# Kernel optimization log

Measured on AMD Instinct MI355X. Metric: run time of the kernel, lower is better.

## Reference

```python
import jax, jax.numpy as jnp
import numpy as np

NUM_CLASSES = 50000
FEAT_DIM = 256
BATCH = 2048
CLAMP_MIN = 1e-12
CLAMP_MAX = 1e12


def setup_inputs() -> dict:
    key = jax.random.key(0)
    k1, k2, k3 = jax.random.split(key, 3)
    x = jax.random.normal(k1, (BATCH, FEAT_DIM), dtype=jnp.float32)
    labels = jax.random.randint(k2, (BATCH,), 0, NUM_CLASSES, dtype=jnp.int64)
    centers = jax.random.normal(k3, (NUM_CLASSES, FEAT_DIM), dtype=jnp.float32)
    class_weights = jnp.ones((NUM_CLASSES,), dtype=jnp.float32)
    return {"x": x, "centers": centers, "class_weights": class_weights, "labels": labels}


def reference(x, centers, class_weights, labels):
    # Original torch code builds a full (B, C) distmat via addmm, masks to the
    # true-class column, multiplies by class weights, clamps to [1e-12, 1e12],
    # and sums / B. Off-mask entries are exactly 0 -> clamped to 1e-12, so they
    # contribute a constant B*(C-1)*1e-12 to the sum. We compute the gathered
    # per-sample distance directly (same math) and add that constant, avoiding
    # the O(B*C) intermediate.
    B = x.shape[0]
    C = centers.shape[0]
    c = centers[labels]                                   # (B, D)
    d = (jnp.sum(x * x, axis=1)
         + jnp.sum(c * c, axis=1)
         - 2.0 * jnp.sum(x * c, axis=1))                  # (B,)
    w = class_weights[labels]                             # (B,)
    on_mask = jnp.clip(d * w, CLAMP_MIN, CLAMP_MAX)       # (B,)
    off_mask_const = jnp.float32(B * (C - 1)) * jnp.float32(CLAMP_MIN)
    loss = (jnp.sum(on_mask) + off_mask_const) / B
    return loss
```

## Files before the change

kernel.cpp:

```cpp
#include <hip/hip_runtime.h>


constexpr int B = 2048;
constexpr int D = 256;
constexpr int C = 50000;

__global__ __launch_bounds__(256) void wcl_persample(
    const float* __restrict__ x, const float* __restrict__ centers,
    const float* __restrict__ cw, const int* __restrict__ labels,
    float* __restrict__ partial) {
  const int lane = threadIdx.x & 63;
  const int wave = (int)((blockIdx.x * blockDim.x + threadIdx.x) >> 6);
  if (wave >= B) return;

  const int lbl = labels[wave];
  const float4 xv = reinterpret_cast<const float4*>(x + (size_t)wave * D)[lane];
  const float4 cv = reinterpret_cast<const float4*>(centers + (size_t)lbl * D)[lane];

  const float xx = xv.x * xv.x + xv.y * xv.y + xv.z * xv.z + xv.w * xv.w;
  const float cc = cv.x * cv.x + cv.y * cv.y + cv.z * cv.z + cv.w * cv.w;
  const float xc = xv.x * cv.x + xv.y * cv.y + xv.z * cv.z + xv.w * cv.w;
  float s = xx + cc - 2.0f * xc;

#pragma unroll
  for (int off = 32; off > 0; off >>= 1) s += __shfl_xor(s, off, 64);

  if (lane == 0) {
    float v = s * cw[lbl];
    v = fminf(fmaxf(v, 1e-12f), 1e12f);
    partial[wave] = v;
  }
}

__global__ __launch_bounds__(256) void wcl_reduce(
    const float* __restrict__ partial, float* __restrict__ out) {
  __shared__ float sdata[4];
  float s = 0.0f;
  for (int i = threadIdx.x; i < B; i += 256) s += partial[i];
#pragma unroll
  for (int off = 32; off > 0; off >>= 1) s += __shfl_xor(s, off, 64);
  const int wid = (int)(threadIdx.x >> 6);
  if ((threadIdx.x & 63) == 0) sdata[wid] = s;
  __syncthreads();
  if (threadIdx.x == 0) {
    const float tot = sdata[0] + sdata[1] + sdata[2] + sdata[3];
    const float off_const = (float)((double)B * (double)(C - 1)) * 1e-12f;
    out[0] = (tot + off_const) / (float)B;
  }
}

extern "C" void kernel_launch(void* const* d_in, const int* in_sizes, int n_in,
                              void* d_out, int out_size, void* d_ws, size_t ws_size,
                              hipStream_t stream) {
  const float* x       = (const float*)d_in[0];
  const float* centers = (const float*)d_in[1];
  const float* cw      = (const float*)d_in[2];
  const int*   labels  = (const int*)d_in[3];
  float* out = (float*)d_out;
  float* partial = (float*)d_ws;

  wcl_persample<<<(B * 64) / 256, 256, 0, stream>>>(x, centers, cw, labels, partial);
  wcl_reduce<<<1, 256, 0, stream>>>(partial, out);
}
```

Before: 13.31 us.

## Fuse per-sample and reduce kernels via cooperative grid sync

Merges the two launches into one cooperative kernel. Each block reduces its 8 samples into a block partial, then a grid-wide sync lets block 0 sum the 256 partials and write the loss. This removes a second kernel launch and the round trip through the partial buffer, at the cost of a grid barrier and the overhead of a cooperative launch.

```diff
diff --git a/kernel.cpp b/kernel.cpp
--- a/kernel.cpp
+++ b/kernel.cpp
@@ -1,51 +1,63 @@
 #include <hip/hip_runtime.h>
+#include <hip/hip_cooperative_groups.h>
+
+namespace cg = cooperative_groups;
 
 
 constexpr int B = 2048;
 constexpr int D = 256;
 constexpr int C = 50000;
+constexpr int BLOCKS = 256;
+constexpr int TPB = 512;
 
-__global__ __launch_bounds__(256) void wcl_persample(
+__global__ __launch_bounds__(TPB) void wcl_fused(
     const float* __restrict__ x, const float* __restrict__ centers,
     const float* __restrict__ cw, const int* __restrict__ labels,
-    float* __restrict__ partial) {
+    float* __restrict__ partial, float* __restrict__ out) {
+  __shared__ float sm[8];
   const int lane = threadIdx.x & 63;
-  const int wave = (int)((blockIdx.x * blockDim.x + threadIdx.x) >> 6);
-  if (wave >= B) return;
+  const int w = (int)(threadIdx.x >> 6);
+  const int s = (int)blockIdx.x * 8 + w;
 
-  const int lbl = labels[wave];
-  const float4 xv = reinterpret_cast<const float4*>(x + (size_t)wave * D)[lane];
+  const int lbl = labels[s];
+  const float4 xv = reinterpret_cast<const float4*>(x + (size_t)s * D)[lane];
   const float4 cv = reinterpret_cast<const float4*>(centers + (size_t)lbl * D)[lane];
 
   const float xx = xv.x * xv.x + xv.y * xv.y + xv.z * xv.z + xv.w * xv.w;
   const float cc = cv.x * cv.x + cv.y * cv.y + cv.z * cv.z + cv.w * cv.w;
   const float xc = xv.x * cv.x + xv.y * cv.y + xv.z * cv.z + xv.w * cv.w;
-  float s = xx + cc - 2.0f * xc;
+  float acc = xx + cc - 2.0f * xc;
 
 #pragma unroll
-  for (int off = 32; off > 0; off >>= 1) s += __shfl_xor(s, off, 64);
+  for (int off = 32; off > 0; off >>= 1) acc += __shfl_xor(acc, off, 64);
 
   if (lane == 0) {
-    float v = s * cw[lbl];
-    v = fminf(fmaxf(v, 1e-12f), 1e12f);
-    partial[wave] = v;
+    float v = acc * cw[lbl];
+    sm[w] = fminf(fmaxf(v, 1e-12f), 1e12f);
   }
-}
-
-__global__ __launch_bounds__(256) void wcl_reduce(
-    const float* __restrict__ partial, float* __restrict__ out) {
-  __shared__ float sdata[4];
-  float s = 0.0f;
-  for (int i = threadIdx.x; i < B; i += 256) s += partial[i];
-#pragma unroll
-  for (int off = 32; off > 0; off >>= 1) s += __shfl_xor(s, off, 64);
-  const int wid = (int)(threadIdx.x >> 6);
-  if ((threadIdx.x & 63) == 0) sdata[wid] = s;
   __syncthreads();
   if (threadIdx.x == 0) {
-    const float tot = sdata[0] + sdata[1] + sdata[2] + sdata[3];
-    const float off_const = (float)((double)B * (double)(C - 1)) * 1e-12f;
-    out[0] = (tot + off_const) / (float)B;
+    float t = 0.0f;
+#pragma unroll
+    for (int i = 0; i < 8; ++i) t += sm[i];
+    partial[blockIdx.x] = t;
+  }
+
+  cg::this_grid().sync();
+
+  if (blockIdx.x == 0) {
+    float p = (threadIdx.x < BLOCKS) ? partial[threadIdx.x] : 0.0f;
+#pragma unroll
+    for (int off = 32; off > 0; off >>= 1) p += __shfl_xor(p, off, 64);
+    if (lane == 0) sm[w] = p;
+    __syncthreads();
+    if (threadIdx.x == 0) {
+      float tot = 0.0f;
+#pragma unroll
+      for (int i = 0; i < 8; ++i) tot += sm[i];
+      const float off_const = 102397952.0f * 1e-12f;
+      out[0] = (tot + off_const) / 2048.0f;
+    }
   }
 }
 
@@ -59,6 +71,8 @@
   float* out = (float*)d_out;
   float* partial = (float*)d_ws;
 
-  wcl_persample<<<(B * 64) / 256, 256, 0, stream>>>(x, centers, cw, labels, partial);
-  wcl_reduce<<<1, 256, 0, stream>>>(partial, out);
+  void* args[] = {(void*)&x, (void*)&centers, (void*)&cw, (void*)&labels,
+                  (void*)&partial, (void*)&out};
+  hipLaunchCooperativeKernel((const void*)wcl_fused, dim3(BLOCKS), dim3(TPB),
+                             args, 0, stream);
 }
```

After: 38.50 us. 189% more time.
